# Optimization experiments

Hardware: AMD Instinct MI355X
Metric: run time of the kernel (lower is better)

## Reference

```python
import jax, jax.numpy as jnp
import numpy as np

N = 16384      # nodes
E = 131072     # edges
D = 768        # in_size = hid_size = out_size (LayerNorm(768) hardcoded)
NT = 4         # num edge types (TypedLinear num_types)
NB = 3         # num bases (basis regularizer)
LN_EPS = 1e-5


def _layernorm(x, gamma, beta):
    mu = jnp.mean(x, axis=-1, keepdims=True)
    var = jnp.mean(jnp.square(x - mu), axis=-1, keepdims=True)
    return (x - mu) * jax.lax.rsqrt(var + LN_EPS) * gamma + beta


def setup_inputs() -> dict:
    key = jax.random.key(0)
    ks = jax.random.split(key, 16)
    s = 0.02  # weight init scale
    return {
        "h": jax.random.normal(ks[0], (N, D), jnp.float32),
        # TypedLinear basis params: W = sum_b coeff[t,b] * basis[b]
        "W_text": jax.random.normal(ks[1], (NB, D, D), jnp.float32) * s,
        "coeff_text": jax.random.normal(ks[2], (NT, NB), jnp.float32),
        "W_user": jax.random.normal(ks[3], (NB, D, D), jnp.float32) * s,
        "coeff_user": jax.random.normal(ks[4], (NT, NB), jnp.float32),
        "W_dst": jax.random.normal(ks[5], (NB, D, D), jnp.float32) * s,
        "coeff_dst": jax.random.normal(ks[6], (NT, NB), jnp.float32),
        "ln_gamma": jnp.ones((D,), jnp.float32),
        "ln_beta": jnp.zeros((D,), jnp.float32),
        "W_lin": jax.random.normal(ks[7], (2 * D, D), jnp.float32) * s,
        "b_lin": jnp.zeros((D,), jnp.float32),
        "src": jax.random.randint(ks[8], (E,), 0, N, dtype=jnp.int32),
        "dst": jax.random.randint(ks[9], (E,), 0, N, dtype=jnp.int32),
        "etype": jax.random.randint(ks[10], (E,), 0, NT, dtype=jnp.int32),
        "hete": jax.random.randint(ks[11], (E,), 0, 2, dtype=jnp.int32),
    }


def reference(h, W_text, coeff_text, W_user, coeff_user, W_dst, coeff_dst,
              ln_gamma, ln_beta, W_lin, b_lin, src, dst, etype, hete):
    # eval mode: dropout = identity
    x = _layernorm(h, ln_gamma, ln_beta)                       # [N, D]
    # Typed-linear via basis decomposition, folded per (type, node): [NT, N, D]
    Ht = jnp.einsum('nd,bdh,tb->tnh', x, W_text, coeff_text)
    Hu = jnp.einsum('nd,bdh,tb->tnh', x, W_user, coeff_user)
    Hd = jnp.einsum('nd,bdh,tb->tnh', x, W_dst, coeff_dst)

    mask = hete > 0                                            # hete vs homo edges
    # per-edge routed source message: [E, D]
    ef = jnp.where(mask[:, None],
                   jax.nn.relu(Ht[etype, src]),
                   jax.nn.relu(Hu[etype, src]))
    # Original concatenates [hete_feat, homo_feat] along edge dim, i.e. a stable
    # permutation putting hete edges first; dst features stay in original order.
    perm = jnp.argsort((~mask).astype(jnp.int32), stable=True)
    feat_perm = ef[perm]                                       # [E, D]
    dfeat = jax.nn.relu(Hd[etype, dst])                        # [E, D]
    m = jnp.concatenate([feat_perm, dfeat], axis=-1)           # [E, 2D]
    # scatter-sum messages to destination nodes
    n = jax.ops.segment_sum(m, dst, num_segments=N)            # [N, 2D]
    z = jax.nn.relu(n @ W_lin + b_lin)                         # [N, D]
    zn = jnp.linalg.norm(z, ord=2, axis=1, keepdims=True)
    zn = jnp.where(zn == 0, jnp.asarray(1.0, z.dtype), zn)
    return z / zn
```

## Files before the change

### kernel.cpp

```cpp
#include <hip/hip_runtime.h>
#include <hip/hip_bf16.h>
#include <cstdint>

static constexpr int N_  = 16384;
static constexpr int E_  = 131072;
static constexpr int D_  = 768;
static constexpr int D2_ = 1536;
static constexpr int DSQ_ = D_ * D_;

static constexpr size_t OFF_XB   = 0;
static constexpr size_t OFF_WCT  = 25165824;
static constexpr size_t OFF_WLT  = 39321600;
static constexpr size_t OFF_NB16 = 41680896;
static constexpr size_t OFF_H4   = 92012544;
static constexpr size_t OFF_ZB   = 92012544;
static constexpr size_t OFF_N1C  = 192675840;
static constexpr size_t OFF_TG   = 217841664;
static constexpr size_t OFF_PAY  = 218365952;
static constexpr size_t OFF_CNT  = 218890240;
static constexpr size_t OFF_BASE = 219152384;
static constexpr size_t OFF_CUR  = 219217936;
static constexpr size_t OFF_BC   = 219283472;
static constexpr size_t OFF_SCAN = 219285520;

typedef __attribute__((ext_vector_type(8))) short short8v;
typedef __attribute__((ext_vector_type(4))) float floatx4;

__device__ __forceinline__ void gld16(const void* g, void* l) {
  __builtin_amdgcn_global_load_lds(
      (const __attribute__((address_space(1))) unsigned int*)g,
      (__attribute__((address_space(3))) unsigned int*)l, 16, 0, 0);
}

__device__ __forceinline__ float b2f(short u) {
  union { unsigned int i; float f; } x;
  x.i = ((unsigned int)(unsigned short)u) << 16;
  return x.f;
}

__device__ __forceinline__ float wave_sum(float v) {
#pragma unroll
  for (int o = 32; o; o >>= 1) v += __shfl_down(v, o, 64);
  return v;
}

__global__ __launch_bounds__(256) void combine_wt_kernel(
    const float* __restrict__ Wt, const float* __restrict__ ct,
    const float* __restrict__ Wu, const float* __restrict__ cu,
    const float* __restrict__ Wd, const float* __restrict__ cd,
    __hip_bfloat16* __restrict__ WcT) {
  __shared__ float tile[64][65];
  int ft = blockIdx.y;
  int f = ft >> 2, t = ft & 3;
  const float* W = (f == 0) ? Wt : ((f == 1) ? Wu : Wd);
  const float* c = ((f == 0) ? ct : ((f == 1) ? cu : cd)) + t * 3;
  int dt = (blockIdx.x / 12) * 64;
  int ht = (blockIdx.x % 12) * 64;
  int tid = threadIdx.x;
#pragma unroll
  for (int jj = 0; jj < 16; jj++) {
    int idx = jj * 256 + tid;
    int rr = idx >> 6, cc = idx & 63;
    size_t i = (size_t)(dt + rr) * D_ + ht + cc;
    tile[rr][cc] = c[0] * W[i] + c[1] * W[DSQ_ + i] + c[2] * W[2 * DSQ_ + i];
  }
  __syncthreads();
#pragma unroll
  for (int jj = 0; jj < 16; jj++) {
    int idx = jj * 256 + tid;
    int hh = idx >> 6, dd = idx & 63;
    WcT[(size_t)ft * DSQ_ + (size_t)(ht + hh) * D_ + dt + dd] =
        __float2bfloat16(tile[dd][hh]);
  }
}

__global__ __launch_bounds__(256) void wlint_kernel(
    const float* __restrict__ W, __hip_bfloat16* __restrict__ WT) {
  int i = blockIdx.x * 256 + threadIdx.x;
  int k = i / D_, h = i % D_;
  WT[(size_t)h * D2_ + k] = __float2bfloat16(W[i]);
}

__global__ __launch_bounds__(256) void ln_kernel(
    const float* __restrict__ h, const float* __restrict__ gamma,
    const float* __restrict__ beta, __hip_bfloat16* __restrict__ x) {
  int v = blockIdx.x, tid = threadIdx.x;
  const float* hr = h + (size_t)v * D_;
  float e0 = hr[tid], e1 = hr[tid + 256], e2 = hr[tid + 512];
  float s = e0 + e1 + e2;
  float q = e0 * e0 + e1 * e1 + e2 * e2;
  __shared__ float red[8];
  __shared__ float mv[2];
  float ws_ = wave_sum(s), wq = wave_sum(q);
  int lane = tid & 63, w = tid >> 6;
  if (lane == 0) { red[w] = ws_; red[4 + w] = wq; }
  __syncthreads();
  if (tid == 0) {
    float S = red[0] + red[1] + red[2] + red[3];
    float Q = red[4] + red[5] + red[6] + red[7];
    float mu = S * (1.0f / D_);
    float var = Q * (1.0f / D_) - mu * mu;
    mv[0] = mu;
    mv[1] = rsqrtf(var + 1e-5f);
  }
  __syncthreads();
  float mu = mv[0], rstd = mv[1];
  __hip_bfloat16* xr = x + (size_t)v * D_;
  xr[tid]       = __float2bfloat16((e0 - mu) * rstd * gamma[tid]       + beta[tid]);
  xr[tid + 256] = __float2bfloat16((e1 - mu) * rstd * gamma[tid + 256] + beta[tid + 256]);
  xr[tid + 512] = __float2bfloat16((e2 - mu) * rstd * gamma[tid + 512] + beta[tid + 512]);
}

__global__ __launch_bounds__(256) void edge_a_kernel(
    const int* __restrict__ hete, const int* __restrict__ dst,
    const int* __restrict__ etype, int* __restrict__ blockcnt,
    int* __restrict__ cnt4) {
  int j = blockIdx.x * 256 + threadIdx.x;
  int flag = hete[j] > 0;
  unsigned long long m = __ballot(flag);
  __shared__ int wsum[4];
  int lane = threadIdx.x & 63, w = threadIdx.x >> 6;
  if (lane == 0) wsum[w] = __popcll(m);
  __syncthreads();
  if (threadIdx.x == 0)
    blockcnt[blockIdx.x] = wsum[0] + wsum[1] + wsum[2] + wsum[3];
  atomicAdd(&cnt4[dst[j] * 4 + etype[j]], 1);
}

__global__ __launch_bounds__(512) void scan_kernel(
    const int* __restrict__ blockcnt, int* __restrict__ scanout) {
  __shared__ int s[512];
  int t = threadIdx.x;
  int v = blockcnt[t];
  s[t] = v;
  __syncthreads();
  for (int o = 1; o < 512; o <<= 1) {
    int add = (t >= o) ? s[t - o] : 0;
    __syncthreads();
    s[t] += add;
    __syncthreads();
  }
  scanout[t] = s[t] - v;
  if (t == 511) scanout[512] = s[511];
}

__global__ __launch_bounds__(256) void edge_b_kernel(
    const int* __restrict__ hete, const int* __restrict__ dst,
    const int* __restrict__ scanout, int* __restrict__ target) {
  int j = blockIdx.x * 256 + threadIdx.x;
  int flag = hete[j] > 0;
  unsigned long long m = __ballot(flag);
  __shared__ int wsum[4];
  int lane = threadIdx.x & 63, w = threadIdx.x >> 6;
  if (lane == 0) wsum[w] = __popcll(m);
  __syncthreads();
  int wpre = 0;
#pragma unroll
  for (int i = 0; i < 4; i++) wpre += (i < w) ? wsum[i] : 0;
  int lpre = __popcll(m & ((1ull << lane) - 1ull));
  int hcum = scanout[blockIdx.x] + wpre + lpre;
  int K = scanout[512];
  int e = flag ? hcum : (K + j - hcum);
  target[j] = dst[e];
}

__global__ __launch_bounds__(1024) void base_scan_kernel(
    const int* __restrict__ cnt4, int* __restrict__ base) {
  __shared__ int s[1024];
  int t = threadIdx.x;
  int loc[16];
  int sum = 0;
#pragma unroll
  for (int i = 0; i < 16; i++) {
    int v = t * 16 + i;
    int d = cnt4[v * 4] + cnt4[v * 4 + 1] + cnt4[v * 4 + 2] + cnt4[v * 4 + 3];
    loc[i] = sum;
    sum += d;
  }
  s[t] = sum;
  __syncthreads();
  for (int o = 1; o < 1024; o <<= 1) {
    int add = (t >= o) ? s[t - o] : 0;
    __syncthreads();
    s[t] += add;
    __syncthreads();
  }
  int pre = t ? s[t - 1] : 0;
#pragma unroll
  for (int i = 0; i < 16; i++) base[t * 16 + i] = pre + loc[i];
  if (t == 1023) base[N_] = s[1023];
}

__global__ __launch_bounds__(256) void edge_sort_kernel(
    const int* __restrict__ target, const int* __restrict__ src,
    const int* __restrict__ etype, const int* __restrict__ hete,
    const int* __restrict__ base, int* __restrict__ cursor,
    int* __restrict__ payload) {
  int j = blockIdx.x * 256 + threadIdx.x;
  int v = target[j];
  int p = base[v] + atomicAdd(&cursor[v], 1);
  int g = ((hete[j] > 0) ? 0 : 4) + etype[j];
  payload[p] = (g << 14) | src[j];
}

template <bool FIRST>
__global__ __launch_bounds__(256) void gather_n1_kernel(
    const __hip_bfloat16* __restrict__ H, const int* __restrict__ base,
    const int* __restrict__ payload, __hip_bfloat16* __restrict__ n1c,
    __hip_bfloat16* __restrict__ nb16, int g0) {
  int wv = threadIdx.x >> 6, lane = threadIdx.x & 63;
  int v = blockIdx.x * 4 + wv;
  int b0 = base[v], b1 = base[v + 1];
  float acc[12];
  if (FIRST) {
#pragma unroll
    for (int i = 0; i < 12; i++) acc[i] = 0.f;
  } else {
    short8v a8 = *(const short8v*)(n1c + (size_t)v * D_ + lane * 8);
    short4  b4 = *(const short4*)(n1c + (size_t)v * D_ + 512 + lane * 4);
#pragma unroll
    for (int i = 0; i < 8; i++) acc[i] = b2f(a8[i]);
    acc[8] = b2f(b4.x); acc[9] = b2f(b4.y);
    acc[10] = b2f(b4.z); acc[11] = b2f(b4.w);
  }
  for (int idx = b0; idx < b1; ++idx) {
    int pl = payload[idx];
    int g = (pl >> 14) - g0;
    if ((unsigned)g > 3u) continue;
    const __hip_bfloat16* row = H + ((size_t)g * N_ + (pl & 16383)) * D_;
    short8v a8 = *(const short8v*)(row + lane * 8);
    short4  b4 = *(const short4*)(row + 512 + lane * 4);
#pragma unroll
    for (int i = 0; i < 8; i++) acc[i] += b2f(a8[i]);
    acc[8] += b2f(b4.x); acc[9] += b2f(b4.y);
    acc[10] += b2f(b4.z); acc[11] += b2f(b4.w);
  }
  __hip_bfloat16 o[12];
#pragma unroll
  for (int i = 0; i < 12; i++) o[i] = __float2bfloat16(acc[i]);
  if (FIRST) {
    *(short8v*)(n1c + (size_t)v * D_ + lane * 8) = *(const short8v*)o;
    *(short4*)(n1c + (size_t)v * D_ + 512 + lane * 4) = *(const short4*)(o + 8);
  } else {
    *(short8v*)(nb16 + (size_t)v * D2_ + lane * 8) = *(const short8v*)o;
    *(short4*)(nb16 + (size_t)v * D2_ + 512 + lane * 4) = *(const short4*)(o + 8);
  }
}

__global__ __launch_bounds__(256) void combine_n2_kernel(
    const __hip_bfloat16* __restrict__ H4, const int* __restrict__ cnt4,
    __hip_bfloat16* __restrict__ nb16) {
  size_t i = ((size_t)blockIdx.x * 256 + threadIdx.x) * 8;
  int v = (int)(i / D_);
  int k = (int)(i % D_);
  float acc[8] = {0.f, 0.f, 0.f, 0.f, 0.f, 0.f, 0.f, 0.f};
#pragma unroll
  for (int t = 0; t < 4; t++) {
    float c = (float)cnt4[v * 4 + t];
    if (c != 0.f) {
      short8v hv = *(const short8v*)(H4 + (size_t)t * N_ * D_ + i);
#pragma unroll
      for (int j = 0; j < 8; j++) acc[j] += c * b2f(hv[j]);
    }
  }
  __hip_bfloat16 o[8];
#pragma unroll
  for (int j = 0; j < 8; j++) o[j] = __float2bfloat16(acc[j]);
  *(short8v*)(nb16 + (size_t)v * D2_ + D_ + k) = *(const short8v*)o;
}

template <bool BIAS>
__global__ __launch_bounds__(256) void gemm_mfma_kernel(
    const __hip_bfloat16* __restrict__ A, const __hip_bfloat16* __restrict__ BT0,
    const float* __restrict__ bias, __hip_bfloat16* __restrict__ C0,
    int M, int N, int K, size_t strideB, size_t strideC) {
  const __hip_bfloat16* BT = BT0 + (size_t)blockIdx.z * strideB;
  __shared__ char lds[32768];
  char* As = lds;
  char* Bs = lds + 16384;
  int tid = threadIdx.x;
  int lane = tid & 63;
  int wv = tid >> 6;
  int wr = wv >> 1, wc = wv & 1;
  int nwg = gridDim.x * gridDim.y;
  int id = blockIdx.y * gridDim.x + blockIdx.x;
  int s = (id & 7) * (nwg >> 3) + (id >> 3);
  int bx = s % gridDim.x, by = s / gridDim.x;
  int row0 = by * 128, col0 = bx * 128;
  int r_ = tid >> 3;
  int s_ = tid & 7;

  floatx4 acc[4][4];
#pragma unroll
  for (int i = 0; i < 4; i++)
#pragma unroll
    for (int j = 0; j < 4; j++) acc[i][j] = floatx4{0.f, 0.f, 0.f, 0.f};

  for (int k0 = 0; k0 < K; k0 += 64) {
    __syncthreads();
#pragma unroll
    for (int is = 0; is < 4; is++) {
      int r = is * 32 + r_;
      int sp = s_ ^ (r & 7);
      gld16(A  + (size_t)(row0 + r) * K + k0 + sp * 8, As + is * 4096 + tid * 16);
      gld16(BT + (size_t)(col0 + r) * K + k0 + sp * 8, Bs + is * 4096 + tid * 16);
    }
    __syncthreads();
#pragma unroll
    for (int kk = 0; kk < 64; kk += 32) {
      int p = (kk >> 3) + (lane >> 4);
      short8v af[4], bf[4];
#pragma unroll
      for (int m = 0; m < 4; m++) {
        int ra = wr * 64 + m * 16 + (lane & 15);
        af[m] = *(const short8v*)(As + ra * 128 + ((p ^ (ra & 7)) << 4));
        int rb = wc * 64 + m * 16 + (lane & 15);
        bf[m] = *(const short8v*)(Bs + rb * 128 + ((p ^ (rb & 7)) << 4));
      }
#pragma unroll
      for (int m = 0; m < 4; m++)
#pragma unroll
        for (int n = 0; n < 4; n++)
          acc[m][n] = __builtin_amdgcn_mfma_f32_16x16x32_bf16(
              af[m], bf[n], acc[m][n], 0, 0, 0);
    }
  }
  __syncthreads();
  char* cs = lds + wv * 8192;
#pragma unroll
  for (int m = 0; m < 4; m++) {
#pragma unroll
    for (int n = 0; n < 4; n++) {
      int c = n * 16 + (lane & 15);
      float bv = BIAS ? bias[col0 + wc * 64 + c] : 0.f;
#pragma unroll
      for (int q = 0; q < 4; q++) {
        int r = m * 16 + (lane >> 4) * 4 + q;
        float v = fmaxf(acc[m][n][q] + bv, 0.f);
        int byte = r * 128 + ((((c >> 3) + r) & 7) << 4) + ((c & 7) << 1);
        *(__hip_bfloat16*)(cs + byte) = __float2bfloat16(v);
      }
    }
  }
  __hip_bfloat16* C = C0 + (size_t)blockIdx.z * strideC;
#pragma unroll
  for (int i = 0; i < 8; i++) {
    int r = i * 8 + (lane >> 3);
    int s8 = lane & 7;
    int p = (s8 + r) & 7;
    short8v v = *(const short8v*)(cs + r * 128 + (p << 4));
    int grow = row0 + wr * 64 + r;
    int gcol = col0 + wc * 64 + s8 * 8;
    *(short8v*)(C + (size_t)grow * N + gcol) = v;
  }
}

__global__ __launch_bounds__(256) void norm_kernel(
    const __hip_bfloat16* __restrict__ z, float* __restrict__ out) {
  int v = blockIdx.x, tid = threadIdx.x;
  float e[4] = {0.f, 0.f, 0.f, 0.f};
  if (tid < 192) {
    short4 a = *(const short4*)(z + (size_t)v * D_ + tid * 4);
    e[0] = b2f(a.x); e[1] = b2f(a.y); e[2] = b2f(a.z); e[3] = b2f(a.w);
  }
  float q = e[0] * e[0] + e[1] * e[1] + e[2] * e[2] + e[3] * e[3];
  __shared__ float red[4];
  __shared__ float sc;
  float wq = wave_sum(q);
  int lane = tid & 63, w = tid >> 6;
  if (lane == 0) red[w] = wq;
  __syncthreads();
  if (tid == 0) {
    float S = red[0] + red[1] + red[2] + red[3];
    float norm = sqrtf(S);
    sc = (norm == 0.f) ? 1.f : (1.f / norm);
  }
  __syncthreads();
  if (tid < 192) {
    float s = sc;
    float4 o = {e[0] * s, e[1] * s, e[2] * s, e[3] * s};
    *(float4*)(out + (size_t)v * D_ + tid * 4) = o;
  }
}

extern "C" void kernel_launch(void* const* d_in, const int* in_sizes, int n_in,
                              void* d_out, int out_size, void* d_ws,
                              size_t ws_size, hipStream_t stream) {
  (void)in_sizes; (void)n_in; (void)out_size; (void)ws_size;
  const float* h      = (const float*)d_in[0];
  const float* W_text = (const float*)d_in[1];
  const float* c_text = (const float*)d_in[2];
  const float* W_user = (const float*)d_in[3];
  const float* c_user = (const float*)d_in[4];
  const float* W_dst  = (const float*)d_in[5];
  const float* c_dst  = (const float*)d_in[6];
  const float* gamma  = (const float*)d_in[7];
  const float* beta   = (const float*)d_in[8];
  const float* W_lin  = (const float*)d_in[9];
  const float* b_lin  = (const float*)d_in[10];
  const int* src      = (const int*)d_in[11];
  const int* dst      = (const int*)d_in[12];
  const int* etype    = (const int*)d_in[13];
  const int* hete     = (const int*)d_in[14];
  float* out          = (float*)d_out;

  char* ws = (char*)d_ws;
  __hip_bfloat16* xb   = (__hip_bfloat16*)(ws + OFF_XB);
  __hip_bfloat16* WcT  = (__hip_bfloat16*)(ws + OFF_WCT);
  __hip_bfloat16* WlT  = (__hip_bfloat16*)(ws + OFF_WLT);
  __hip_bfloat16* nb16 = (__hip_bfloat16*)(ws + OFF_NB16);
  __hip_bfloat16* H4   = (__hip_bfloat16*)(ws + OFF_H4);
  __hip_bfloat16* zbuf = (__hip_bfloat16*)(ws + OFF_ZB);
  __hip_bfloat16* n1c  = (__hip_bfloat16*)(ws + OFF_N1C);
  int* target   = (int*)(ws + OFF_TG);
  int* payload  = (int*)(ws + OFF_PAY);
  int* cnt4     = (int*)(ws + OFF_CNT);
  int* base     = (int*)(ws + OFF_BASE);
  int* cursor   = (int*)(ws + OFF_CUR);
  int* blockcnt = (int*)(ws + OFF_BC);
  int* scanout  = (int*)(ws + OFF_SCAN);

  hipMemsetAsync(cnt4, 0, (size_t)N_ * 4 * 4, stream);
  hipMemsetAsync(cursor, 0, (size_t)N_ * 4, stream);

  combine_wt_kernel<<<dim3(144, 12), 256, 0, stream>>>(
      W_text, c_text, W_user, c_user, W_dst, c_dst, WcT);
  wlint_kernel<<<(D2_ * D_) / 256, 256, 0, stream>>>(W_lin, WlT);
  ln_kernel<<<N_, 256, 0, stream>>>(h, gamma, beta, xb);
  edge_a_kernel<<<E_ / 256, 256, 0, stream>>>(hete, dst, etype, blockcnt, cnt4);
  scan_kernel<<<1, 512, 0, stream>>>(blockcnt, scanout);
  edge_b_kernel<<<E_ / 256, 256, 0, stream>>>(hete, dst, scanout, target);
  base_scan_kernel<<<1, 1024, 0, stream>>>(cnt4, base);
  edge_sort_kernel<<<E_ / 256, 256, 0, stream>>>(target, src, etype, hete,
                                                 base, cursor, payload);

  const size_t HSTRIDE = (size_t)N_ * D_;
  const dim3 ggrid(D_ / 128, N_ / 128, 4);

  gemm_mfma_kernel<false><<<ggrid, 256, 0, stream>>>(
      xb, WcT + (size_t)8 * DSQ_, nullptr, H4, N_, D_, D_, DSQ_, HSTRIDE);
  combine_n2_kernel<<<(N_ * D_) / (256 * 8), 256, 0, stream>>>(H4, cnt4, nb16);

  gemm_mfma_kernel<false><<<ggrid, 256, 0, stream>>>(
      xb, WcT, nullptr, H4, N_, D_, D_, DSQ_, HSTRIDE);
  gather_n1_kernel<true><<<N_ / 4, 256, 0, stream>>>(H4, base, payload, n1c,
                                                     nb16, 0);
  gemm_mfma_kernel<false><<<ggrid, 256, 0, stream>>>(
      xb, WcT + (size_t)4 * DSQ_, nullptr, H4, N_, D_, D_, DSQ_, HSTRIDE);
  gather_n1_kernel<false><<<N_ / 4, 256, 0, stream>>>(H4, base, payload, n1c,
                                                      nb16, 4);

  gemm_mfma_kernel<true><<<dim3(D_ / 128, N_ / 128, 1), 256, 0, stream>>>(
      nb16, WlT, b_lin, zbuf, N_, D_, D2_, 0, 0);
  norm_kernel<<<N_, 256, 0, stream>>>(zbuf, out);
}
```

Measured before the change: 492.3 us.

## Project onto 3 bases instead of 4 typed weights and combine per edge

Instead of folding the basis coefficients into four per-type weight matrices and running four GEMMs per family, the GEMMs now project onto the three raw basis matrices. The per-type coefficient combination and ReLU move into the gather and combine kernels. This cuts GEMM work and the size of the intermediate buffer by a quarter, but each edge in the gather now reads three basis rows instead of one and does extra FMAs. The GEMM tile swizzle now also spans the z dimension, and the ReLU becomes a template flag so the basis projections are stored without it.

```diff
diff --git a/kernel.cpp b/kernel.cpp
--- a/kernel.cpp
+++ b/kernel.cpp
@@ -9,10 +9,10 @@
 static constexpr int DSQ_ = D_ * D_;
 
 static constexpr size_t OFF_XB   = 0;
-static constexpr size_t OFF_WCT  = 25165824;
+static constexpr size_t OFF_WBT  = 25165824;
 static constexpr size_t OFF_WLT  = 39321600;
 static constexpr size_t OFF_NB16 = 41680896;
-static constexpr size_t OFF_H4   = 92012544;
+static constexpr size_t OFF_Y3   = 92012544;
 static constexpr size_t OFF_ZB   = 92012544;
 static constexpr size_t OFF_N1C  = 192675840;
 static constexpr size_t OFF_TG   = 217841664;
@@ -44,16 +44,13 @@
   return v;
 }
 
-__global__ __launch_bounds__(256) void combine_wt_kernel(
-    const float* __restrict__ Wt, const float* __restrict__ ct,
-    const float* __restrict__ Wu, const float* __restrict__ cu,
-    const float* __restrict__ Wd, const float* __restrict__ cd,
-    __hip_bfloat16* __restrict__ WcT) {
+__global__ __launch_bounds__(256) void wbasis_t_kernel(
+    const float* __restrict__ Wt, const float* __restrict__ Wu,
+    const float* __restrict__ Wd, __hip_bfloat16* __restrict__ WbT) {
   __shared__ float tile[64][65];
-  int ft = blockIdx.y;
-  int f = ft >> 2, t = ft & 3;
-  const float* W = (f == 0) ? Wt : ((f == 1) ? Wu : Wd);
-  const float* c = ((f == 0) ? ct : ((f == 1) ? cu : cd)) + t * 3;
+  int fb = blockIdx.y;
+  int f = fb / 3, b = fb % 3;
+  const float* W = ((f == 0) ? Wt : ((f == 1) ? Wu : Wd)) + (size_t)b * DSQ_;
   int dt = (blockIdx.x / 12) * 64;
   int ht = (blockIdx.x % 12) * 64;
   int tid = threadIdx.x;
@@ -61,15 +58,14 @@
   for (int jj = 0; jj < 16; jj++) {
     int idx = jj * 256 + tid;
     int rr = idx >> 6, cc = idx & 63;
-    size_t i = (size_t)(dt + rr) * D_ + ht + cc;
-    tile[rr][cc] = c[0] * W[i] + c[1] * W[DSQ_ + i] + c[2] * W[2 * DSQ_ + i];
+    tile[rr][cc] = W[(size_t)(dt + rr) * D_ + ht + cc];
   }
   __syncthreads();
 #pragma unroll
   for (int jj = 0; jj < 16; jj++) {
     int idx = jj * 256 + tid;
     int hh = idx >> 6, dd = idx & 63;
-    WcT[(size_t)ft * DSQ_ + (size_t)(ht + hh) * D_ + dt + dd] =
+    WbT[(size_t)fb * DSQ_ + (size_t)(ht + hh) * D_ + dt + dd] =
         __float2bfloat16(tile[dd][hh]);
   }
 }
@@ -205,12 +201,16 @@
 
 template <bool FIRST>
 __global__ __launch_bounds__(256) void gather_n1_kernel(
-    const __hip_bfloat16* __restrict__ H, const int* __restrict__ base,
-    const int* __restrict__ payload, __hip_bfloat16* __restrict__ n1c,
-    __hip_bfloat16* __restrict__ nb16, int g0) {
+    const __hip_bfloat16* __restrict__ Y, const float* __restrict__ coeff,
+    const int* __restrict__ base, const int* __restrict__ payload,
+    __hip_bfloat16* __restrict__ n1c, __hip_bfloat16* __restrict__ nb16,
+    int g0) {
   int wv = threadIdx.x >> 6, lane = threadIdx.x & 63;
   int v = blockIdx.x * 4 + wv;
   int b0 = base[v], b1 = base[v + 1];
+  float cf[12];
+#pragma unroll
+  for (int i = 0; i < 12; i++) cf[i] = coeff[i];
   float acc[12];
   if (FIRST) {
 #pragma unroll
@@ -223,17 +223,26 @@
     acc[8] = b2f(b4.x); acc[9] = b2f(b4.y);
     acc[10] = b2f(b4.z); acc[11] = b2f(b4.w);
   }
+  const size_t YS = (size_t)N_ * D_;
   for (int idx = b0; idx < b1; ++idx) {
     int pl = payload[idx];
-    int g = (pl >> 14) - g0;
-    if ((unsigned)g > 3u) continue;
-    const __hip_bfloat16* row = H + ((size_t)g * N_ + (pl & 16383)) * D_;
-    short8v a8 = *(const short8v*)(row + lane * 8);
-    short4  b4 = *(const short4*)(row + 512 + lane * 4);
-#pragma unroll
-    for (int i = 0; i < 8; i++) acc[i] += b2f(a8[i]);
-    acc[8] += b2f(b4.x); acc[9] += b2f(b4.y);
-    acc[10] += b2f(b4.z); acc[11] += b2f(b4.w);
+    int t = (pl >> 14) - g0;
+    if ((unsigned)t > 3u) continue;
+    float c0 = cf[t * 3], c1 = cf[t * 3 + 1], c2 = cf[t * 3 + 2];
+    const __hip_bfloat16* r0 = Y + (size_t)(pl & 16383) * D_;
+    short8v a0 = *(const short8v*)(r0 + lane * 8);
+    short8v a1 = *(const short8v*)(r0 + YS + lane * 8);
+    short8v a2 = *(const short8v*)(r0 + 2 * YS + lane * 8);
+    short4  b0v = *(const short4*)(r0 + 512 + lane * 4);
+    short4  b1v = *(const short4*)(r0 + YS + 512 + lane * 4);
+    short4  b2v = *(const short4*)(r0 + 2 * YS + 512 + lane * 4);
+#pragma unroll
+    for (int i = 0; i < 8; i++)
+      acc[i] += fmaxf(c0 * b2f(a0[i]) + c1 * b2f(a1[i]) + c2 * b2f(a2[i]), 0.f);
+    acc[8]  += fmaxf(c0 * b2f(b0v.x) + c1 * b2f(b1v.x) + c2 * b2f(b2v.x), 0.f);
+    acc[9]  += fmaxf(c0 * b2f(b0v.y) + c1 * b2f(b1v.y) + c2 * b2f(b2v.y), 0.f);
+    acc[10] += fmaxf(c0 * b2f(b0v.z) + c1 * b2f(b1v.z) + c2 * b2f(b2v.z), 0.f);
+    acc[11] += fmaxf(c0 * b2f(b0v.w) + c1 * b2f(b1v.w) + c2 * b2f(b2v.w), 0.f);
   }
   __hip_bfloat16 o[12];
 #pragma unroll
@@ -248,19 +257,29 @@
 }
 
 __global__ __launch_bounds__(256) void combine_n2_kernel(
-    const __hip_bfloat16* __restrict__ H4, const int* __restrict__ cnt4,
-    __hip_bfloat16* __restrict__ nb16) {
+    const __hip_bfloat16* __restrict__ Y, const float* __restrict__ cd,
+    const int* __restrict__ cnt4, __hip_bfloat16* __restrict__ nb16) {
   size_t i = ((size_t)blockIdx.x * 256 + threadIdx.x) * 8;
   int v = (int)(i / D_);
   int k = (int)(i % D_);
+  const size_t YS = (size_t)N_ * D_;
+  short8v y0 = *(const short8v*)(Y + i);
+  short8v y1 = *(const short8v*)(Y + YS + i);
+  short8v y2 = *(const short8v*)(Y + 2 * YS + i);
+  float f0[8], f1[8], f2[8];
+#pragma unroll
+  for (int j = 0; j < 8; j++) {
+    f0[j] = b2f(y0[j]); f1[j] = b2f(y1[j]); f2[j] = b2f(y2[j]);
+  }
   float acc[8] = {0.f, 0.f, 0.f, 0.f, 0.f, 0.f, 0.f, 0.f};
 #pragma unroll
   for (int t = 0; t < 4; t++) {
     float c = (float)cnt4[v * 4 + t];
     if (c != 0.f) {
-      short8v hv = *(const short8v*)(H4 + (size_t)t * N_ * D_ + i);
-#pragma unroll
-      for (int j = 0; j < 8; j++) acc[j] += c * b2f(hv[j]);
+      float d0 = cd[t * 3], d1 = cd[t * 3 + 1], d2 = cd[t * 3 + 2];
+#pragma unroll
+      for (int j = 0; j < 8; j++)
+        acc[j] += c * fmaxf(d0 * f0[j] + d1 * f1[j] + d2 * f2[j], 0.f);
     }
   }
   __hip_bfloat16 o[8];
@@ -269,12 +288,11 @@
   *(short8v*)(nb16 + (size_t)v * D2_ + D_ + k) = *(const short8v*)o;
 }
 
-template <bool BIAS>
+template <bool BIAS, bool RELU>
 __global__ __launch_bounds__(256) void gemm_mfma_kernel(
     const __hip_bfloat16* __restrict__ A, const __hip_bfloat16* __restrict__ BT0,
     const float* __restrict__ bias, __hip_bfloat16* __restrict__ C0,
     int M, int N, int K, size_t strideB, size_t strideC) {
-  const __hip_bfloat16* BT = BT0 + (size_t)blockIdx.z * strideB;
   __shared__ char lds[32768];
   char* As = lds;
   char* Bs = lds + 16384;
@@ -282,10 +300,15 @@
   int lane = tid & 63;
   int wv = tid >> 6;
   int wr = wv >> 1, wc = wv & 1;
-  int nwg = gridDim.x * gridDim.y;
-  int id = blockIdx.y * gridDim.x + blockIdx.x;
+  int gx = gridDim.x, gz = gridDim.z;
+  int nwg = gx * gridDim.y * gz;
+  int id = (blockIdx.z * gridDim.y + blockIdx.y) * gx + blockIdx.x;
   int s = (id & 7) * (nwg >> 3) + (id >> 3);
-  int bx = s % gridDim.x, by = s / gridDim.x;
+  int bx = s % gx;
+  int rem = s / gx;
+  int z = rem % gz;
+  int by = rem / gz;
+  const __hip_bfloat16* BT = BT0 + (size_t)z * strideB;
   int row0 = by * 128, col0 = bx * 128;
   int r_ = tid >> 3;
   int s_ = tid & 7;
@@ -336,13 +359,14 @@
 #pragma unroll
       for (int q = 0; q < 4; q++) {
         int r = m * 16 + (lane >> 4) * 4 + q;
-        float v = fmaxf(acc[m][n][q] + bv, 0.f);
+        float v = acc[m][n][q] + bv;
+        if (RELU) v = fmaxf(v, 0.f);
         int byte = r * 128 + ((((c >> 3) + r) & 7) << 4) + ((c & 7) << 1);
         *(__hip_bfloat16*)(cs + byte) = __float2bfloat16(v);
       }
     }
   }
-  __hip_bfloat16* C = C0 + (size_t)blockIdx.z * strideC;
+  __hip_bfloat16* C = C0 + (size_t)z * strideC;
 #pragma unroll
   for (int i = 0; i < 8; i++) {
     int r = i * 8 + (lane >> 3);
@@ -406,10 +430,10 @@
 
   char* ws = (char*)d_ws;
   __hip_bfloat16* xb   = (__hip_bfloat16*)(ws + OFF_XB);
-  __hip_bfloat16* WcT  = (__hip_bfloat16*)(ws + OFF_WCT);
+  __hip_bfloat16* WbT  = (__hip_bfloat16*)(ws + OFF_WBT);
   __hip_bfloat16* WlT  = (__hip_bfloat16*)(ws + OFF_WLT);
   __hip_bfloat16* nb16 = (__hip_bfloat16*)(ws + OFF_NB16);
-  __hip_bfloat16* H4   = (__hip_bfloat16*)(ws + OFF_H4);
+  __hip_bfloat16* Y3   = (__hip_bfloat16*)(ws + OFF_Y3);
   __hip_bfloat16* zbuf = (__hip_bfloat16*)(ws + OFF_ZB);
   __hip_bfloat16* n1c  = (__hip_bfloat16*)(ws + OFF_N1C);
   int* target   = (int*)(ws + OFF_TG);
@@ -423,8 +447,7 @@
   hipMemsetAsync(cnt4, 0, (size_t)N_ * 4 * 4, stream);
   hipMemsetAsync(cursor, 0, (size_t)N_ * 4, stream);
 
-  combine_wt_kernel<<<dim3(144, 12), 256, 0, stream>>>(
-      W_text, c_text, W_user, c_user, W_dst, c_dst, WcT);
+  wbasis_t_kernel<<<dim3(144, 9), 256, 0, stream>>>(W_text, W_user, W_dst, WbT);
   wlint_kernel<<<(D2_ * D_) / 256, 256, 0, stream>>>(W_lin, WlT);
   ln_kernel<<<N_, 256, 0, stream>>>(h, gamma, beta, xb);
   edge_a_kernel<<<E_ / 256, 256, 0, stream>>>(hete, dst, etype, blockcnt, cnt4);
@@ -435,22 +458,22 @@
                                                  base, cursor, payload);
 
   const size_t HSTRIDE = (size_t)N_ * D_;
-  const dim3 ggrid(D_ / 128, N_ / 128, 4);
-
-  gemm_mfma_kernel<false><<<ggrid, 256, 0, stream>>>(
-      xb, WcT + (size_t)8 * DSQ_, nullptr, H4, N_, D_, D_, DSQ_, HSTRIDE);
-  combine_n2_kernel<<<(N_ * D_) / (256 * 8), 256, 0, stream>>>(H4, cnt4, nb16);
-
-  gemm_mfma_kernel<false><<<ggrid, 256, 0, stream>>>(
-      xb, WcT, nullptr, H4, N_, D_, D_, DSQ_, HSTRIDE);
-  gather_n1_kernel<true><<<N_ / 4, 256, 0, stream>>>(H4, base, payload, n1c,
-                                                     nb16, 0);
-  gemm_mfma_kernel<false><<<ggrid, 256, 0, stream>>>(
-      xb, WcT + (size_t)4 * DSQ_, nullptr, H4, N_, D_, D_, DSQ_, HSTRIDE);
-  gather_n1_kernel<false><<<N_ / 4, 256, 0, stream>>>(H4, base, payload, n1c,
-                                                      nb16, 4);
-
-  gemm_mfma_kernel<true><<<dim3(D_ / 128, N_ / 128, 1), 256, 0, stream>>>(
+  const dim3 ggrid(D_ / 128, N_ / 128, 3);
+
+  gemm_mfma_kernel<false, false><<<ggrid, 256, 0, stream>>>(
+      xb, WbT + (size_t)6 * DSQ_, nullptr, Y3, N_, D_, D_, DSQ_, HSTRIDE);
+  combine_n2_kernel<<<(N_ * D_) / (256 * 8), 256, 0, stream>>>(Y3, c_dst,
+                                                               cnt4, nb16);
+  gemm_mfma_kernel<false, false><<<ggrid, 256, 0, stream>>>(
+      xb, WbT, nullptr, Y3, N_, D_, D_, DSQ_, HSTRIDE);
+  gather_n1_kernel<true><<<N_ / 4, 256, 0, stream>>>(Y3, c_text, base, payload,
+                                                     n1c, nb16, 0);
+  gemm_mfma_kernel<false, false><<<ggrid, 256, 0, stream>>>(
+      xb, WbT + (size_t)3 * DSQ_, nullptr, Y3, N_, D_, D_, DSQ_, HSTRIDE);
+  gather_n1_kernel<false><<<N_ / 4, 256, 0, stream>>>(Y3, c_user, base,
+                                                      payload, n1c, nb16, 4);
+
+  gemm_mfma_kernel<true, true><<<dim3(D_ / 128, N_ / 128, 1), 256, 0, stream>>>(
       nb16, WlT, b_lin, zbuf, N_, D_, D2_, 0, 0);
   norm_kernel<<<N_, 256, 0, stream>>>(zbuf, out);
 }
```

Result: faster. 478.4 us (-2.8%).
